# Kernel optimization log

Measured on AMD Instinct MI355X. Metric: run time of the kernel, lower is better.

The kernel has to match this reference:

```python
import jax, jax.numpy as jnp
import numpy as np

BS, SEQ, IN, H = 16, 1024, 512, 512


def setup_inputs() -> dict:
    key = jax.random.key(0)
    ks = jax.random.split(key, 10)
    std = 1.0 / np.sqrt(H)
    u = lambda k, shape: jax.random.uniform(k, shape, jnp.float32, -std, std)
    return {
        "x": jax.random.normal(ks[0], (BS, SEQ, IN), jnp.float32),
        # input projection fc: input_size -> hidden_size
        "Wfc": u(ks[1], (IN, H)),
        "bfc": u(ks[2], (H,)),
        # cell 1 (main hidden stream h): tree of matmuls + gated elementwise
        "W1x": u(ks[3], (2 * H, H)),  # layer-0 cells see duplicated features (2H)
        "W1h": u(ks[4], (H, H)),
        "W1g": u(ks[5], (H, H)),
        # cell 2 (second hidden stream c)
        "W2x": u(ks[6], (2 * H, H)),
        "W2h": u(ks[7], (H, H)),
        "W2g": u(ks[8], (H, H)),
    }


def reference(x, Wfc, bfc, W1x, W1h, W1g, W2x, W2h, W2g):
    bs = x.shape[0]
    # layer-0 input prep: fc projection then feature duplication (cat([x,x],dim=2))
    xp = x @ Wfc + bfc                      # [bs, seq, H]
    xp = jnp.concatenate([xp, xp], axis=-1)  # [bs, seq, 2H]
    xs = jnp.swapaxes(xp, 0, 1)             # [seq, bs, 2H] for scan over time

    h0 = jnp.zeros((bs, H), x.dtype)
    c0 = jnp.zeros((bs, H), x.dtype)

    def step(carry, x_t):
        h, c = carry  # hidden streams x2, x3 fed to each evolved cell
        h_new = jnp.tanh(x_t @ W1x + h @ W1h + jax.nn.sigmoid(c @ W1g) * h)
        c_new = jax.nn.sigmoid(x_t @ W2x + c @ W2h) * jnp.tanh(h @ W2g)
        return (h_new, c_new), h_new  # hidden_seq collects stream 0

    (h_fin, c_fin), hseq = jax.lax.scan(step, (h0, c0), xs)
    out = jnp.swapaxes(hseq, 0, 1)  # batch_first: [bs, seq, H]
    # final hidden states: [num_layers*(1), bs, H] per main stream
    return out, h_fin[None], c_fin[None]
```

## Files before the change

kernel.cpp:

```cpp
#include <hip/hip_runtime.h>


typedef unsigned short u16;
typedef unsigned int   u32;
typedef __attribute__((ext_vector_type(8))) short s8v;
typedef __attribute__((ext_vector_type(4))) float f4v;

__device__ __forceinline__ u16 f2bf_rne(float f){
  u32 u = __float_as_uint(f);
  u32 r = u + 0x7fffu + ((u >> 16) & 1u);
  return (u16)(r >> 16);
}
__device__ __forceinline__ float bf2f(u16 h){ return __uint_as_float(((u32)h) << 16); }
__device__ __forceinline__ f4v MFMA(s8v a, s8v b, f4v c){
  return __builtin_amdgcn_mfma_f32_16x16x32_bf16(a, b, c, 0, 0, 0);
}
__device__ __forceinline__ float sigmoidf_(float x){ return 1.0f / (1.0f + __expf(-x)); }
__device__ __forceinline__ float tanh_fast(float x){
  float e = __expf(2.0f * x);
  return 1.0f - 2.0f / (e + 1.0f);
}

template<bool CC> __device__ __forceinline__ s8v ld16(const u16* p){
  s8v r;
  if (CC) asm volatile("global_load_dwordx4 %0, %1, off sc0 sc1" : "=v"(r) : "v"(p));
  else    asm volatile("global_load_dwordx4 %0, %1, off"         : "=v"(r) : "v"(p));
  return r;
}
template<bool CC> __device__ __forceinline__ void st2(u16* p, u32 v){
  if (CC) asm volatile("global_store_short %0, %1, off sc0 sc1" :: "v"(p), "v"(v) : "memory");
  else    asm volatile("global_store_short %0, %1, off"         :: "v"(p), "v"(v) : "memory");
}
__device__ __forceinline__ void store_dword_cc(u32* p, u32 v){
  asm volatile("global_store_dword %0, %1, off sc0 sc1" :: "v"(p), "v"(v) : "memory");
}
__device__ __forceinline__ void store_dword_plain_wait(u32* p, u32 v){
  asm volatile("global_store_dword %0, %1, off\n\ts_waitcnt vmcnt(0)"
               :: "v"(p), "v"(v) : "memory");
}
__device__ __forceinline__ u32 load_dword_plain_wait(const u32* p){
  u32 r;
  asm volatile("global_load_dword %0, %1, off\n\ts_waitcnt vmcnt(0)"
               : "=v"(r) : "v"(p));
  return r;
}

#define SEQT 1024
#define NWG  16
#define PROT 16

static const size_t OFF_U1  = 0;
static const size_t OFF_U2  = 33554432;
static const size_t OFF_WCT = OFF_U2 + 16777216;
static const size_t OFF_ST  = OFF_WCT;
static const size_t OFF_WT  = OFF_WCT + 1048576;
static const size_t OFF_BC  = OFF_WT + 2097152;
static const size_t OFF_FL  = OFF_BC + 4096;
static const size_t OFF_TOK = OFF_FL + 65536;
static const size_t OFF_PRS = OFF_TOK + 4096;
static const size_t OFF_CTL = OFF_PRS + 4096;
static const size_t OFF_CN  = OFF_CTL + 4096;

__global__ void wcombk(const float* __restrict__ Wfc, const float* __restrict__ W1x,
                       const float* __restrict__ W2x, u16* __restrict__ Wct){
  __shared__ float A[16][17], B[16][17];
  const float* Wx = blockIdx.z ? W2x : W1x;
  int i0 = blockIdx.y * 16, n0 = blockIdx.x * 16;
  int tx = threadIdx.x, ty = threadIdx.y;
  float acc = 0.f;
  for (int kc = 0; kc < 512; kc += 16){
    A[ty][tx] = Wfc[(size_t)(i0 + ty) * 512 + kc + tx];
    B[ty][tx] = Wx[(size_t)(kc + ty) * 512 + n0 + tx]
              + Wx[(size_t)(kc + ty + 512) * 512 + n0 + tx];
    __syncthreads();
    #pragma unroll
    for (int kk = 0; kk < 16; ++kk) acc += A[ty][kk] * B[kk][tx];
    __syncthreads();
  }
  Wct[(size_t)(blockIdx.z * 512 + n0 + tx) * 512 + i0 + ty] = f2bf_rne(acc);
}

__global__ void bcombk(const float* __restrict__ bfc, const float* __restrict__ W1x,
                       const float* __restrict__ W2x, float* __restrict__ bc){
  int n = blockIdx.x * 256 + threadIdx.x;
  const float* Wx = (n < 512) ? W1x : W2x;
  int nl = n & 511;
  float acc = 0.f;
  for (int k = 0; k < 512; ++k)
    acc += bfc[k] * (Wx[(size_t)k * 512 + nl] + Wx[(size_t)(k + 512) * 512 + nl]);
  bc[n] = acc;
}

__global__ void wtk(const float* __restrict__ A, const float* __restrict__ B,
                    const float* __restrict__ C, const float* __restrict__ D,
                    u16* __restrict__ Wt){
  __shared__ float tile[32][33];
  const float* src = (blockIdx.z == 0) ? A : (blockIdx.z == 1) ? B
                    : (blockIdx.z == 2) ? C : D;
  int n0 = blockIdx.x * 32, k0 = blockIdx.y * 32;
  for (int i = threadIdx.y; i < 32; i += 8)
    tile[i][threadIdx.x] = src[(size_t)(k0 + i) * 512 + n0 + threadIdx.x];
  __syncthreads();
  for (int i = threadIdx.y; i < 32; i += 8)
    Wt[(size_t)blockIdx.z * 262144 + (size_t)(n0 + i) * 512 + k0 + threadIdx.x]
        = f2bf_rne(tile[threadIdx.x][i]);
}

__global__ __launch_bounds__(256) void gemmk(
    const float* __restrict__ x, const u16* __restrict__ Wct,
    const float* __restrict__ bc, float* __restrict__ U1, u16* __restrict__ U2){
  int l = threadIdx.x & 63, w = threadIdx.x >> 6;
  int lr = l & 15, lk = l >> 4;
  int m0 = blockIdx.y * 128 + (w & 1) * 64;
  int n0 = blockIdx.x * 64 + (w >> 1) * 32;
  f4v acc[4][2] = {};
  for (int ks = 0; ks < 16; ++ks){
    int k0 = ks * 32 + lk * 8;
    s8v bh0 = *(const s8v*)(Wct + (size_t)(n0 + lr) * 512 + k0);
    s8v bh1 = *(const s8v*)(Wct + (size_t)(n0 + 16 + lr) * 512 + k0);
    #pragma unroll
    for (int mi = 0; mi < 4; ++mi){
      const float* xp = x + (size_t)(m0 + mi * 16 + lr) * 512 + k0;
      f4v v0 = *(const f4v*)xp;
      f4v v1 = *(const f4v*)(xp + 4);
      s8v ah, al;
      #pragma unroll
      for (int j = 0; j < 4; ++j){
        { u32 u = __float_as_uint(v0[j]); ah[j] = (short)(u >> 16);
          float lof = v0[j] - __uint_as_float(u & 0xffff0000u);
          al[j] = (short)(__float_as_uint(lof) >> 16); }
        { u32 u = __float_as_uint(v1[j]); ah[j + 4] = (short)(u >> 16);
          float lof = v1[j] - __uint_as_float(u & 0xffff0000u);
          al[j + 4] = (short)(__float_as_uint(lof) >> 16); }
      }
      acc[mi][0] = MFMA(ah, bh0, acc[mi][0]);
      acc[mi][0] = MFMA(al, bh0, acc[mi][0]);
      acc[mi][1] = MFMA(ah, bh1, acc[mi][1]);
      acc[mi][1] = MFMA(al, bh1, acc[mi][1]);
    }
  }
  #pragma unroll
  for (int mi = 0; mi < 4; ++mi)
    #pragma unroll
    for (int ni = 0; ni < 2; ++ni){
      int n = n0 + ni * 16 + lr;
      float badd = bc[n];
      #pragma unroll
      for (int j = 0; j < 4; ++j){
        int r = m0 + mi * 16 + lk * 4 + j;
        int b = r >> 10, t = r & 1023;
        size_t oi = (size_t)(t * 16 + b) * 512;
        float v = acc[mi][ni][j] + badd;
        if (n < 512) U1[oi + n] = v;
        else         U2[oi + n - 512] = f2bf_rne(v);
      }
    }
}

template<bool CC>
__device__ __forceinline__ void scan_loop(
    int wg, int tid,
    const float* __restrict__ U1, const u16* __restrict__ U2,
    const u16* __restrict__ Wt, u16* __restrict__ st,
    u32* __restrict__ flags, u32* __restrict__ cnt,
    float* __restrict__ out, float* xg, float* xt){
  const int w = tid >> 6, l = tid & 63;
  const int lr = l & 15, lk = l >> 4;
  const int ncol0 = wg * 32 + lr;

  s8v bf0[16], bf1[16];
  {
    const u16* Wm = Wt + (size_t)w * (512 * 512);
    #pragma unroll
    for (int ks = 0; ks < 16; ++ks){
      bf0[ks] = *(const s8v*)(Wm + (size_t)ncol0 * 512 + ks * 32 + lk * 8);
      bf1[ks] = *(const s8v*)(Wm + (size_t)(ncol0 + 16) * 512 + ks * 32 + lk * 8);
    }
  }
  const bool useH = (w == 0) || (w == 3);
  float hp0[4] = {0, 0, 0, 0}, hp1[4] = {0, 0, 0, 0};
  long guard = 0;

  float un0[4], un1[4], uc0[4], uc1[4];
  u32   ur0[4], ur1[4];
  if (w == 0){
    #pragma unroll
    for (int j = 0; j < 4; ++j){
      size_t ro = (size_t)(lk * 4 + j) * 512;
      un0[j] = U1[ro + ncol0];
      un1[j] = U1[ro + ncol0 + 16];
    }
  } else if (w == 2){
    #pragma unroll
    for (int j = 0; j < 4; ++j){
      size_t ro = (size_t)(lk * 4 + j) * 512;
      ur0[j] = U2[ro + ncol0];
      ur1[j] = U2[ro + ncol0 + 16];
    }
  }

  for (int t = 0; t < SEQT; ++t){
    if (t > 0){
      if (CC){
        const u32* fl = flags + (size_t)(t - 1) * NWG;
        for (;;){
          u32 v = 1u;
          if (l < NWG) v = __hip_atomic_load(fl + l, __ATOMIC_RELAXED, __HIP_MEMORY_SCOPE_AGENT);
          if (__all(v != 0u)) break;
          if (++guard > 1000000L) break;
        }
      } else {
        if (w == 0){
          for (;;){
            u32 v = 0;
            if (l == 0)
              v = __hip_atomic_fetch_add(cnt + (t - 1), 0x10000u, __ATOMIC_RELAXED,
                                         __HIP_MEMORY_SCOPE_WORKGROUP);
            v = __builtin_amdgcn_readfirstlane(v);
            if ((v & 0xffffu) >= NWG) break;
            if (++guard > 8000000L) break;
          }
        }
        __syncthreads();
      }
      __builtin_amdgcn_sched_barrier(0);
    }
    u16* rb = st + (size_t)(t & (PROT - 1)) * 32768 + (useH ? 0 : 16384);
    s8v ah[16], al[16];
    {
      u16* bhp = rb + lr * 512 + lk * 8;
      u16* blp = rb + 8192 + lr * 512 + lk * 8;
      #pragma unroll
      for (int ks = 0; ks < 16; ++ks){
        ah[ks] = ld16<CC>(bhp + ks * 32);
        al[ks] = ld16<CC>(blp + ks * 32);
      }
    }
    asm volatile("s_waitcnt vmcnt(0)" ::: "memory");
    __builtin_amdgcn_sched_barrier(0);

    if (w == 0){
      #pragma unroll
      for (int j = 0; j < 4; ++j){ uc0[j] = un0[j]; uc1[j] = un1[j]; }
    } else if (w == 2){
      #pragma unroll
      for (int j = 0; j < 4; ++j){
        uc0[j] = __uint_as_float(ur0[j] << 16);
        uc1[j] = __uint_as_float(ur1[j] << 16);
      }
    }

    f4v a0 = {0, 0, 0, 0}, a1 = {0, 0, 0, 0};
    f4v b0 = {0, 0, 0, 0}, b1 = {0, 0, 0, 0};
    #pragma unroll
    for (int ks = 0; ks < 16; ++ks){
      a0 = MFMA(ah[ks], bf0[ks], a0);
      a1 = MFMA(ah[ks], bf1[ks], a1);
      b0 = MFMA(al[ks], bf0[ks], b0);
      b1 = MFMA(al[ks], bf1[ks], b1);
    }
    #pragma unroll
    for (int j = 0; j < 4; ++j){ a0[j] += b0[j]; a1[j] += b1[j]; }

    if (w == 1){
      #pragma unroll
      for (int j = 0; j < 4; ++j){
        xg[(0 * 16 + lk * 4 + j) * 16 + lr] = sigmoidf_(a0[j]);
        xg[(1 * 16 + lk * 4 + j) * 16 + lr] = sigmoidf_(a1[j]);
      }
    } else if (w == 3){
      #pragma unroll
      for (int j = 0; j < 4; ++j){
        xt[(0 * 16 + lk * 4 + j) * 16 + lr] = tanh_fast(a0[j]);
        xt[(1 * 16 + lk * 4 + j) * 16 + lr] = tanh_fast(a1[j]);
      }
    }
    __syncthreads();
    u16* wb = st + (size_t)((t + 1) & (PROT - 1)) * 32768;
    const int tn = (t + 1 < SEQT) ? t + 1 : t;
    float hn0v[4], hn1v[4], cn0v[4], cn1v[4];
    if (w == 0){
      #pragma unroll
      for (int j = 0; j < 4; ++j){
        int b = lk * 4 + j;
        float hn0 = tanh_fast(uc0[j] + a0[j] + xg[(0 * 16 + b) * 16 + lr] * hp0[j]);
        float hn1 = tanh_fast(uc1[j] + a1[j] + xg[(1 * 16 + b) * 16 + lr] * hp1[j]);
        hp0[j] = hn0; hp1[j] = hn1;
        hn0v[j] = hn0; hn1v[j] = hn1;
        u32 u0 = __float_as_uint(hn0), u1 = __float_as_uint(hn1);
        int bi = b * 512;
        st2<CC>(wb + bi + ncol0,      u0 >> 16);
        st2<CC>(wb + bi + ncol0 + 16, u1 >> 16);
        float lo0 = hn0 - __uint_as_float(u0 & 0xffff0000u);
        float lo1 = hn1 - __uint_as_float(u1 & 0xffff0000u);
        st2<CC>(wb + 8192 + bi + ncol0,      __float_as_uint(lo0) >> 16);
        st2<CC>(wb + 8192 + bi + ncol0 + 16, __float_as_uint(lo1) >> 16);
      }
      #pragma unroll
      for (int j = 0; j < 4; ++j){
        size_t ro = (size_t)(tn * 16 + lk * 4 + j) * 512;
        un0[j] = U1[ro + ncol0];
        un1[j] = U1[ro + ncol0 + 16];
      }
      asm volatile("s_waitcnt vmcnt(8)" ::: "memory");
    } else if (w == 2){
      #pragma unroll
      for (int j = 0; j < 4; ++j){
        int b = lk * 4 + j;
        float cn0 = sigmoidf_(uc0[j] + a0[j]) * xt[(0 * 16 + b) * 16 + lr];
        float cn1 = sigmoidf_(uc1[j] + a1[j]) * xt[(1 * 16 + b) * 16 + lr];
        cn0v[j] = cn0; cn1v[j] = cn1;
        u32 u0 = __float_as_uint(cn0), u1 = __float_as_uint(cn1);
        int bi = b * 512;
        st2<CC>(wb + 16384 + bi + ncol0,      u0 >> 16);
        st2<CC>(wb + 16384 + bi + ncol0 + 16, u1 >> 16);
        float lo0 = cn0 - __uint_as_float(u0 & 0xffff0000u);
        float lo1 = cn1 - __uint_as_float(u1 & 0xffff0000u);
        st2<CC>(wb + 24576 + bi + ncol0,      __float_as_uint(lo0) >> 16);
        st2<CC>(wb + 24576 + bi + ncol0 + 16, __float_as_uint(lo1) >> 16);
      }
      #pragma unroll
      for (int j = 0; j < 4; ++j){
        size_t ro = (size_t)(tn * 16 + lk * 4 + j) * 512;
        ur0[j] = U2[ro + ncol0];
        ur1[j] = U2[ro + ncol0 + 16];
      }
      asm volatile("s_waitcnt vmcnt(8)" ::: "memory");
    }
    __syncthreads();
    if (tid == 0){
      if (CC) store_dword_cc(flags + (size_t)t * NWG + wg, 1u);
      else    __hip_atomic_fetch_add(cnt + t, 1u, __ATOMIC_RELAXED,
                                     __HIP_MEMORY_SCOPE_WORKGROUP);
    }
    if (w == 0){
      #pragma unroll
      for (int j = 0; j < 4; ++j){
        int b = lk * 4 + j;
        size_t ob = (size_t)b * (SEQT * 512) + (size_t)t * 512;
        out[ob + ncol0]      = hn0v[j];
        out[ob + ncol0 + 16] = hn1v[j];
        if (t == SEQT - 1){
          out[8388608 + (size_t)b * 512 + ncol0]      = hn0v[j];
          out[8388608 + (size_t)b * 512 + ncol0 + 16] = hn1v[j];
        }
      }
    } else if (w == 2 && t == SEQT - 1){
      #pragma unroll
      for (int j = 0; j < 4; ++j){
        int b = lk * 4 + j;
        out[8396800 + (size_t)b * 512 + ncol0]      = cn0v[j];
        out[8396800 + (size_t)b * 512 + ncol0 + 16] = cn1v[j];
      }
    }
  }
}

__global__ __launch_bounds__(256, 1) void recurk(
    const float* __restrict__ U1, const u16* __restrict__ U2,
    const u16* __restrict__ Wt, u16* __restrict__ st,
    u32* __restrict__ flags, u32* __restrict__ cnt,
    u32* __restrict__ tok, u32* __restrict__ prs,
    u32* __restrict__ ctl, float* __restrict__ out){
  const int tid = threadIdx.x;
  __shared__ int slot_sh, mode_sh;
  __shared__ float xg[2 * 16 * 16], xt[2 * 16 * 16];
  u32* cntp  = ctl;
  u32* modep = ctl + 16;

  if (tid == 0){
    int s = -1;
    u32 xcc;
    asm volatile("s_getreg_b32 %0, hwreg(HW_REG_XCC_ID)" : "=s"(xcc));
    if ((xcc & 0xfu) == 0u)
      s = (int)__hip_atomic_fetch_add(cntp, 1u, __ATOMIC_RELAXED,
                                      __HIP_MEMORY_SCOPE_AGENT);
    slot_sh = s;
  }
  __syncthreads();
  const int slot = slot_sh;

  if (tid == 0){
    if (slot >= 0 && slot < NWG){
      store_dword_plain_wait(tok + slot * 16, 0x5A5A0000u + (u32)slot);
      __hip_atomic_store(prs + slot * 16, 1u, __ATOMIC_RELAXED,
                         __HIP_MEMORY_SCOPE_AGENT);
    }
    if (blockIdx.x == 0){
      long g = 0;
      for (;;){
        u32 c = __hip_atomic_load(cntp, __ATOMIC_RELAXED, __HIP_MEMORY_SCOPE_AGENT);
        if (c >= NWG) break;
        if (++g > 2000000L){ atomicCAS(modep, 0u, 2u); break; }
      }
    }
    if (slot == 0){
      bool ok = true;
      long g = 0;
      for (int s2 = 1; s2 < NWG && ok; ++s2){
        for (;;){
          u32 p = __hip_atomic_load(prs + s2 * 16, __ATOMIC_RELAXED,
                                    __HIP_MEMORY_SCOPE_AGENT);
          if (p) break;
          if (++g > 5000000L){ ok = false; break; }
        }
      }
      if (ok){
        for (int s2 = 1; s2 < NWG; ++s2){
          u32 v = load_dword_plain_wait(tok + s2 * 16);
          if (v != 0x5A5A0000u + (u32)s2){ ok = false; break; }
        }
      }
      atomicCAS(modep, 0u, ok ? 1u : 3u);
    }
    long g = 0;
    u32 m;
    for (;;){
      m = __hip_atomic_load(modep, __ATOMIC_RELAXED, __HIP_MEMORY_SCOPE_AGENT);
      if (m) break;
      if (++g > 50000000L){ m = 3u; break; }
    }
    mode_sh = (int)m;
  }
  __syncthreads();
  const int mode = mode_sh;

  int wg; bool part;
  if (mode == 2){ wg = blockIdx.x; part = (wg < NWG); }
  else          { wg = slot;       part = (slot >= 0 && slot < NWG); }
  if (!part) return;

  if (mode == 1) scan_loop<false>(wg, tid, U1, U2, Wt, st, flags, cnt, out, xg, xt);
  else           scan_loop<true >(wg, tid, U1, U2, Wt, st, flags, cnt, out, xg, xt);
}

extern "C" void kernel_launch(void* const* d_in, const int* in_sizes, int n_in,
                              void* d_out, int out_size, void* d_ws, size_t ws_size,
                              hipStream_t stream){
  const float* x   = (const float*)d_in[0];
  const float* Wfc = (const float*)d_in[1];
  const float* bfc = (const float*)d_in[2];
  const float* W1x = (const float*)d_in[3];
  const float* W1h = (const float*)d_in[4];
  const float* W1g = (const float*)d_in[5];
  const float* W2x = (const float*)d_in[6];
  const float* W2h = (const float*)d_in[7];
  const float* W2g = (const float*)d_in[8];

  char* ws = (char*)d_ws;
  float* U1   = (float*)(ws + OFF_U1);
  u16*   U2   = (u16*)  (ws + OFF_U2);
  u16*   Wct  = (u16*)  (ws + OFF_WCT);
  u16*   st   = (u16*)  (ws + OFF_ST);
  u16*   Wt   = (u16*)  (ws + OFF_WT);
  float* bc   = (float*)(ws + OFF_BC);
  u32*   flags= (u32*)  (ws + OFF_FL);
  u32*   tok  = (u32*)  (ws + OFF_TOK);
  u32*   prs  = (u32*)  (ws + OFF_PRS);
  u32*   ctl  = (u32*)  (ws + OFF_CTL);
  u32*   cnt  = (u32*)  (ws + OFF_CN);
  float* out  = (float*)d_out;

  hipMemsetAsync(ws + OFF_FL, 0, 65536 + 4096 + 4096 + 4096 + 4096, stream);

  wcombk<<<dim3(32, 32, 2), dim3(16, 16), 0, stream>>>(Wfc, W1x, W2x, Wct);
  bcombk<<<dim3(4), dim3(256), 0, stream>>>(bfc, W1x, W2x, bc);
  wtk   <<<dim3(16, 16, 4), dim3(32, 8), 0, stream>>>(W1h, W1g, W2h, W2g, Wt);
  gemmk <<<dim3(16, 128), dim3(256), 0, stream>>>(x, Wct, bc, U1, U2);
  hipMemsetAsync(ws + OFF_ST, 0, 1048576, stream);
  recurk<<<dim3(256), dim3(256), 0, stream>>>(U1, U2, Wt, st, flags, cnt, tok, prs, ctl, out);
}
```

Measured before the change: 6.445 ms.

## Split per-stream readiness flags and drop end-of-step block barrier in fast scan

```diff
diff --git a/kernel.cpp b/kernel.cpp
--- a/kernel.cpp
+++ b/kernel.cpp
@@ -60,6 +60,8 @@
 static const size_t OFF_PRS = OFF_TOK + 4096;
 static const size_t OFF_CTL = OFF_PRS + 4096;
 static const size_t OFF_CN  = OFF_CTL + 4096;
+static const size_t OFF_HF2 = OFF_CN + 4096;
+static const size_t OFF_CF2 = OFF_HF2 + 1048576;
 
 __global__ void wcombk(const float* __restrict__ Wfc, const float* __restrict__ W1x,
                        const float* __restrict__ W2x, u16* __restrict__ Wct){
@@ -157,12 +159,11 @@
     }
 }
 
-template<bool CC>
-__device__ __forceinline__ void scan_loop(
+__device__ __forceinline__ void scan_fast(
     int wg, int tid,
     const float* __restrict__ U1, const u16* __restrict__ U2,
     const u16* __restrict__ Wt, u16* __restrict__ st,
-    u32* __restrict__ flags, u32* __restrict__ cnt,
+    u32* __restrict__ hfl, u32* __restrict__ cfl,
     float* __restrict__ out, float* xg, float* xt){
   const int w = tid >> 6, l = tid & 63;
   const int lr = l & 15, lk = l >> 4;
@@ -178,8 +179,8 @@
     }
   }
   const bool useH = (w == 0) || (w == 3);
+  u32* myfl = useH ? hfl : cfl;
   float hp0[4] = {0, 0, 0, 0}, hp1[4] = {0, 0, 0, 0};
-  long guard = 0;
 
   float un0[4], un1[4], uc0[4], uc1[4];
   u32   ur0[4], ur1[4];
@@ -201,27 +202,17 @@
 
   for (int t = 0; t < SEQT; ++t){
     if (t > 0){
-      if (CC){
-        const u32* fl = flags + (size_t)(t - 1) * NWG;
-        for (;;){
-          u32 v = 1u;
-          if (l < NWG) v = __hip_atomic_load(fl + l, __ATOMIC_RELAXED, __HIP_MEMORY_SCOPE_AGENT);
-          if (__all(v != 0u)) break;
-          if (++guard > 1000000L) break;
+      u32* fl = myfl + (size_t)(t - 1) * (NWG * 16);
+      u32 seen = (l < NWG) ? 0u : 1u;
+      int g2 = 0;
+      for (;;){
+        if (!seen){
+          u32 v = __hip_atomic_fetch_add(fl + l * 16, 0x10000u,
+                                         __ATOMIC_RELAXED, __HIP_MEMORY_SCOPE_WORKGROUP);
+          if ((v & 0xffffu) != 0u) seen = 1u;
         }
-      } else {
-        if (w == 0){
-          for (;;){
-            u32 v = 0;
-            if (l == 0)
-              v = __hip_atomic_fetch_add(cnt + (t - 1), 0x10000u, __ATOMIC_RELAXED,
-                                         __HIP_MEMORY_SCOPE_WORKGROUP);
-            v = __builtin_amdgcn_readfirstlane(v);
-            if ((v & 0xffffu) >= NWG) break;
-            if (++guard > 8000000L) break;
-          }
-        }
-        __syncthreads();
+        if (__all(seen != 0u)) break;
+        if (++g2 > 2000000) break;
       }
       __builtin_amdgcn_sched_barrier(0);
     }
@@ -232,8 +223,8 @@
       u16* blp = rb + 8192 + lr * 512 + lk * 8;
       #pragma unroll
       for (int ks = 0; ks < 16; ++ks){
-        ah[ks] = ld16<CC>(bhp + ks * 32);
-        al[ks] = ld16<CC>(blp + ks * 32);
+        ah[ks] = ld16<false>(bhp + ks * 32);
+        al[ks] = ld16<false>(blp + ks * 32);
       }
     }
     asm volatile("s_waitcnt vmcnt(0)" ::: "memory");
@@ -262,39 +253,40 @@
     #pragma unroll
     for (int j = 0; j < 4; ++j){ a0[j] += b0[j]; a1[j] += b1[j]; }
 
+    const int par = t & 1;
     if (w == 1){
       #pragma unroll
       for (int j = 0; j < 4; ++j){
-        xg[(0 * 16 + lk * 4 + j) * 16 + lr] = sigmoidf_(a0[j]);
-        xg[(1 * 16 + lk * 4 + j) * 16 + lr] = sigmoidf_(a1[j]);
+        xg[((par * 2 + 0) * 16 + lk * 4 + j) * 16 + lr] = sigmoidf_(a0[j]);
+        xg[((par * 2 + 1) * 16 + lk * 4 + j) * 16 + lr] = sigmoidf_(a1[j]);
       }
     } else if (w == 3){
       #pragma unroll
       for (int j = 0; j < 4; ++j){
-        xt[(0 * 16 + lk * 4 + j) * 16 + lr] = tanh_fast(a0[j]);
-        xt[(1 * 16 + lk * 4 + j) * 16 + lr] = tanh_fast(a1[j]);
+        xt[((par * 2 + 0) * 16 + lk * 4 + j) * 16 + lr] = tanh_fast(a0[j]);
+        xt[((par * 2 + 1) * 16 + lk * 4 + j) * 16 + lr] = tanh_fast(a1[j]);
       }
     }
     __syncthreads();
     u16* wb = st + (size_t)((t + 1) & (PROT - 1)) * 32768;
     const int tn = (t + 1 < SEQT) ? t + 1 : t;
-    float hn0v[4], hn1v[4], cn0v[4], cn1v[4];
     if (w == 0){
+      float hn0v[4], hn1v[4];
       #pragma unroll
       for (int j = 0; j < 4; ++j){
         int b = lk * 4 + j;
-        float hn0 = tanh_fast(uc0[j] + a0[j] + xg[(0 * 16 + b) * 16 + lr] * hp0[j]);
-        float hn1 = tanh_fast(uc1[j] + a1[j] + xg[(1 * 16 + b) * 16 + lr] * hp1[j]);
+        float hn0 = tanh_fast(uc0[j] + a0[j] + xg[((par * 2 + 0) * 16 + b) * 16 + lr] * hp0[j]);
+        float hn1 = tanh_fast(uc1[j] + a1[j] + xg[((par * 2 + 1) * 16 + b) * 16 + lr] * hp1[j]);
         hp0[j] = hn0; hp1[j] = hn1;
         hn0v[j] = hn0; hn1v[j] = hn1;
         u32 u0 = __float_as_uint(hn0), u1 = __float_as_uint(hn1);
         int bi = b * 512;
-        st2<CC>(wb + bi + ncol0,      u0 >> 16);
-        st2<CC>(wb + bi + ncol0 + 16, u1 >> 16);
+        st2<false>(wb + bi + ncol0,      u0 >> 16);
+        st2<false>(wb + bi + ncol0 + 16, u1 >> 16);
         float lo0 = hn0 - __uint_as_float(u0 & 0xffff0000u);
         float lo1 = hn1 - __uint_as_float(u1 & 0xffff0000u);
-        st2<CC>(wb + 8192 + bi + ncol0,      __float_as_uint(lo0) >> 16);
-        st2<CC>(wb + 8192 + bi + ncol0 + 16, __float_as_uint(lo1) >> 16);
+        st2<false>(wb + 8192 + bi + ncol0,      __float_as_uint(lo0) >> 16);
+        st2<false>(wb + 8192 + bi + ncol0 + 16, __float_as_uint(lo1) >> 16);
       }
       #pragma unroll
       for (int j = 0; j < 4; ++j){
@@ -303,37 +295,9 @@
         un1[j] = U1[ro + ncol0 + 16];
       }
       asm volatile("s_waitcnt vmcnt(8)" ::: "memory");
-    } else if (w == 2){
-      #pragma unroll
-      for (int j = 0; j < 4; ++j){
-        int b = lk * 4 + j;
-        float cn0 = sigmoidf_(uc0[j] + a0[j]) * xt[(0 * 16 + b) * 16 + lr];
-        float cn1 = sigmoidf_(uc1[j] + a1[j]) * xt[(1 * 16 + b) * 16 + lr];
-        cn0v[j] = cn0; cn1v[j] = cn1;
-        u32 u0 = __float_as_uint(cn0), u1 = __float_as_uint(cn1);
-        int bi = b * 512;
-        st2<CC>(wb + 16384 + bi + ncol0,      u0 >> 16);
-        st2<CC>(wb + 16384 + bi + ncol0 + 16, u1 >> 16);
-        float lo0 = cn0 - __uint_as_float(u0 & 0xffff0000u);
-        float lo1 = cn1 - __uint_as_float(u1 & 0xffff0000u);
-        st2<CC>(wb + 24576 + bi + ncol0,      __float_as_uint(lo0) >> 16);
-        st2<CC>(wb + 24576 + bi + ncol0 + 16, __float_as_uint(lo1) >> 16);
-      }
-      #pragma unroll
-      for (int j = 0; j < 4; ++j){
-        size_t ro = (size_t)(tn * 16 + lk * 4 + j) * 512;
-        ur0[j] = U2[ro + ncol0];
-        ur1[j] = U2[ro + ncol0 + 16];
-      }
-      asm volatile("s_waitcnt vmcnt(8)" ::: "memory");
-    }
-    __syncthreads();
-    if (tid == 0){
-      if (CC) store_dword_cc(flags + (size_t)t * NWG + wg, 1u);
-      else    __hip_atomic_fetch_add(cnt + t, 1u, __ATOMIC_RELAXED,
-                                     __HIP_MEMORY_SCOPE_WORKGROUP);
-    }
-    if (w == 0){
+      if (l == 0)
+        __hip_atomic_fetch_add(hfl + (size_t)t * (NWG * 16) + wg * 16, 1u,
+                               __ATOMIC_RELAXED, __HIP_MEMORY_SCOPE_WORKGROUP);
       #pragma unroll
       for (int j = 0; j < 4; ++j){
         int b = lk * 4 + j;
@@ -345,6 +309,182 @@
           out[8388608 + (size_t)b * 512 + ncol0 + 16] = hn1v[j];
         }
       }
+    } else if (w == 2){
+      float cn0v[4], cn1v[4];
+      #pragma unroll
+      for (int j = 0; j < 4; ++j){
+        int b = lk * 4 + j;
+        float cn0 = sigmoidf_(uc0[j] + a0[j]) * xt[((par * 2 + 0) * 16 + b) * 16 + lr];
+        float cn1 = sigmoidf_(uc1[j] + a1[j]) * xt[((par * 2 + 1) * 16 + b) * 16 + lr];
+        cn0v[j] = cn0; cn1v[j] = cn1;
+        u32 u0 = __float_as_uint(cn0), u1 = __float_as_uint(cn1);
+        int bi = b * 512;
+        st2<false>(wb + 16384 + bi + ncol0,      u0 >> 16);
+        st2<false>(wb + 16384 + bi + ncol0 + 16, u1 >> 16);
+        float lo0 = cn0 - __uint_as_float(u0 & 0xffff0000u);
+        float lo1 = cn1 - __uint_as_float(u1 & 0xffff0000u);
+        st2<false>(wb + 24576 + bi + ncol0,      __float_as_uint(lo0) >> 16);
+        st2<false>(wb + 24576 + bi + ncol0 + 16, __float_as_uint(lo1) >> 16);
+      }
+      #pragma unroll
+      for (int j = 0; j < 4; ++j){
+        size_t ro = (size_t)(tn * 16 + lk * 4 + j) * 512;
+        ur0[j] = U2[ro + ncol0];
+        ur1[j] = U2[ro + ncol0 + 16];
+      }
+      asm volatile("s_waitcnt vmcnt(8)" ::: "memory");
+      if (l == 0)
+        __hip_atomic_fetch_add(cfl + (size_t)t * (NWG * 16) + wg * 16, 1u,
+                               __ATOMIC_RELAXED, __HIP_MEMORY_SCOPE_WORKGROUP);
+      if (t == SEQT - 1){
+        #pragma unroll
+        for (int j = 0; j < 4; ++j){
+          int b = lk * 4 + j;
+          out[8396800 + (size_t)b * 512 + ncol0]      = cn0v[j];
+          out[8396800 + (size_t)b * 512 + ncol0 + 16] = cn1v[j];
+        }
+      }
+    }
+  }
+}
+
+__device__ __forceinline__ void scan_cc(
+    int wg, int tid,
+    const float* __restrict__ U1, const u16* __restrict__ U2,
+    const u16* __restrict__ Wt, u16* __restrict__ st,
+    u32* __restrict__ flags, float* __restrict__ out, float* xg, float* xt){
+  const int w = tid >> 6, l = tid & 63;
+  const int lr = l & 15, lk = l >> 4;
+  const int ncol0 = wg * 32 + lr;
+  s8v bf0[16], bf1[16];
+  {
+    const u16* Wm = Wt + (size_t)w * (512 * 512);
+    #pragma unroll
+    for (int ks = 0; ks < 16; ++ks){
+      bf0[ks] = *(const s8v*)(Wm + (size_t)ncol0 * 512 + ks * 32 + lk * 8);
+      bf1[ks] = *(const s8v*)(Wm + (size_t)(ncol0 + 16) * 512 + ks * 32 + lk * 8);
+    }
+  }
+  const bool useH = (w == 0) || (w == 3);
+  float hp0[4] = {0, 0, 0, 0}, hp1[4] = {0, 0, 0, 0};
+  long guard = 0;
+  for (int t = 0; t < SEQT; ++t){
+    float uu0[4], uu1[4];
+    if (w == 0){
+      #pragma unroll
+      for (int j = 0; j < 4; ++j){
+        size_t ro = (size_t)(t * 16 + lk * 4 + j) * 512;
+        uu0[j] = U1[ro + ncol0];
+        uu1[j] = U1[ro + ncol0 + 16];
+      }
+    } else if (w == 2){
+      #pragma unroll
+      for (int j = 0; j < 4; ++j){
+        size_t ro = (size_t)(t * 16 + lk * 4 + j) * 512;
+        uu0[j] = bf2f(U2[ro + ncol0]);
+        uu1[j] = bf2f(U2[ro + ncol0 + 16]);
+      }
+    }
+    if (t > 0){
+      const u32* fl = flags + (size_t)(t - 1) * NWG;
+      for (;;){
+        u32 v = 1u;
+        if (l < NWG) v = __hip_atomic_load(fl + l, __ATOMIC_RELAXED, __HIP_MEMORY_SCOPE_AGENT);
+        if (__all(v != 0u)) break;
+        if (++guard > 1000000L) break;
+      }
+      __builtin_amdgcn_sched_barrier(0);
+    }
+    u16* rb = st + (size_t)(t & (PROT - 1)) * 32768 + (useH ? 0 : 16384);
+    s8v ah[16], al[16];
+    {
+      u16* bhp = rb + lr * 512 + lk * 8;
+      u16* blp = rb + 8192 + lr * 512 + lk * 8;
+      #pragma unroll
+      for (int ks = 0; ks < 16; ++ks){
+        ah[ks] = ld16<true>(bhp + ks * 32);
+        al[ks] = ld16<true>(blp + ks * 32);
+      }
+    }
+    asm volatile("s_waitcnt vmcnt(0)" ::: "memory");
+    __builtin_amdgcn_sched_barrier(0);
+    f4v a0 = {0, 0, 0, 0}, a1 = {0, 0, 0, 0};
+    f4v b0 = {0, 0, 0, 0}, b1 = {0, 0, 0, 0};
+    #pragma unroll
+    for (int ks = 0; ks < 16; ++ks){
+      a0 = MFMA(ah[ks], bf0[ks], a0);
+      a1 = MFMA(ah[ks], bf1[ks], a1);
+      b0 = MFMA(al[ks], bf0[ks], b0);
+      b1 = MFMA(al[ks], bf1[ks], b1);
+    }
+    #pragma unroll
+    for (int j = 0; j < 4; ++j){ a0[j] += b0[j]; a1[j] += b1[j]; }
+    if (w == 1){
+      #pragma unroll
+      for (int j = 0; j < 4; ++j){
+        xg[(0 * 16 + lk * 4 + j) * 16 + lr] = sigmoidf_(a0[j]);
+        xg[(1 * 16 + lk * 4 + j) * 16 + lr] = sigmoidf_(a1[j]);
+      }
+    } else if (w == 3){
+      #pragma unroll
+      for (int j = 0; j < 4; ++j){
+        xt[(0 * 16 + lk * 4 + j) * 16 + lr] = tanh_fast(a0[j]);
+        xt[(1 * 16 + lk * 4 + j) * 16 + lr] = tanh_fast(a1[j]);
+      }
+    }
+    __syncthreads();
+    u16* wb = st + (size_t)((t + 1) & (PROT - 1)) * 32768;
+    float hn0v[4], hn1v[4], cn0v[4], cn1v[4];
+    if (w == 0){
+      #pragma unroll
+      for (int j = 0; j < 4; ++j){
+        int b = lk * 4 + j;
+        float hn0 = tanh_fast(uu0[j] + a0[j] + xg[(0 * 16 + b) * 16 + lr] * hp0[j]);
+        float hn1 = tanh_fast(uu1[j] + a1[j] + xg[(1 * 16 + b) * 16 + lr] * hp1[j]);
+        hp0[j] = hn0; hp1[j] = hn1;
+        hn0v[j] = hn0; hn1v[j] = hn1;
+        u32 u0 = __float_as_uint(hn0), u1 = __float_as_uint(hn1);
+        int bi = b * 512;
+        st2<true>(wb + bi + ncol0,      u0 >> 16);
+        st2<true>(wb + bi + ncol0 + 16, u1 >> 16);
+        float lo0 = hn0 - __uint_as_float(u0 & 0xffff0000u);
+        float lo1 = hn1 - __uint_as_float(u1 & 0xffff0000u);
+        st2<true>(wb + 8192 + bi + ncol0,      __float_as_uint(lo0) >> 16);
+        st2<true>(wb + 8192 + bi + ncol0 + 16, __float_as_uint(lo1) >> 16);
+      }
+      asm volatile("s_waitcnt vmcnt(0)" ::: "memory");
+    } else if (w == 2){
+      #pragma unroll
+      for (int j = 0; j < 4; ++j){
+        int b = lk * 4 + j;
+        float cn0 = sigmoidf_(uu0[j] + a0[j]) * xt[(0 * 16 + b) * 16 + lr];
+        float cn1 = sigmoidf_(uu1[j] + a1[j]) * xt[(1 * 16 + b) * 16 + lr];
+        cn0v[j] = cn0; cn1v[j] = cn1;
+        u32 u0 = __float_as_uint(cn0), u1 = __float_as_uint(cn1);
+        int bi = b * 512;
+        st2<true>(wb + 16384 + bi + ncol0,      u0 >> 16);
+        st2<true>(wb + 16384 + bi + ncol0 + 16, u1 >> 16);
+        float lo0 = cn0 - __uint_as_float(u0 & 0xffff0000u);
+        float lo1 = cn1 - __uint_as_float(u1 & 0xffff0000u);
+        st2<true>(wb + 24576 + bi + ncol0,      __float_as_uint(lo0) >> 16);
+        st2<true>(wb + 24576 + bi + ncol0 + 16, __float_as_uint(lo1) >> 16);
+      }
+      asm volatile("s_waitcnt vmcnt(0)" ::: "memory");
+    }
+    __syncthreads();
+    if (tid == 0) store_dword_cc(flags + (size_t)t * NWG + wg, 1u);
+    if (w == 0){
+      #pragma unroll
+      for (int j = 0; j < 4; ++j){
+        int b = lk * 4 + j;
+        size_t ob = (size_t)b * (SEQT * 512) + (size_t)t * 512;
+        out[ob + ncol0]      = hn0v[j];
+        out[ob + ncol0 + 16] = hn1v[j];
+        if (t == SEQT - 1){
+          out[8388608 + (size_t)b * 512 + ncol0]      = hn0v[j];
+          out[8388608 + (size_t)b * 512 + ncol0 + 16] = hn1v[j];
+        }
+      }
     } else if (w == 2 && t == SEQT - 1){
       #pragma unroll
       for (int j = 0; j < 4; ++j){
@@ -359,12 +499,12 @@
 __global__ __launch_bounds__(256, 1) void recurk(
     const float* __restrict__ U1, const u16* __restrict__ U2,
     const u16* __restrict__ Wt, u16* __restrict__ st,
-    u32* __restrict__ flags, u32* __restrict__ cnt,
+    u32* __restrict__ flags, u32* __restrict__ hfl, u32* __restrict__ cfl,
     u32* __restrict__ tok, u32* __restrict__ prs,
     u32* __restrict__ ctl, float* __restrict__ out){
   const int tid = threadIdx.x;
   __shared__ int slot_sh, mode_sh;
-  __shared__ float xg[2 * 16 * 16], xt[2 * 16 * 16];
+  __shared__ float xg[4 * 16 * 16], xt[4 * 16 * 16];
   u32* cntp  = ctl;
   u32* modep = ctl + 16;
 
@@ -430,8 +570,8 @@
   else          { wg = slot;       part = (slot >= 0 && slot < NWG); }
   if (!part) return;
 
-  if (mode == 1) scan_loop<false>(wg, tid, U1, U2, Wt, st, flags, cnt, out, xg, xt);
-  else           scan_loop<true >(wg, tid, U1, U2, Wt, st, flags, cnt, out, xg, xt);
+  if (mode == 1) scan_fast(wg, tid, U1, U2, Wt, st, hfl, cfl, out, xg, xt);
+  else           scan_cc (wg, tid, U1, U2, Wt, st, flags, out, xg, xt);
 }
 
 extern "C" void kernel_launch(void* const* d_in, const int* in_sizes, int n_in,
@@ -458,15 +598,17 @@
   u32*   tok  = (u32*)  (ws + OFF_TOK);
   u32*   prs  = (u32*)  (ws + OFF_PRS);
   u32*   ctl  = (u32*)  (ws + OFF_CTL);
-  u32*   cnt  = (u32*)  (ws + OFF_CN);
+  u32*   hfl  = (u32*)  (ws + OFF_HF2);
+  u32*   cfl  = (u32*)  (ws + OFF_CF2);
   float* out  = (float*)d_out;
 
   hipMemsetAsync(ws + OFF_FL, 0, 65536 + 4096 + 4096 + 4096 + 4096, stream);
+  hipMemsetAsync(ws + OFF_HF2, 0, 2097152, stream);
 
   wcombk<<<dim3(32, 32, 2), dim3(16, 16), 0, stream>>>(Wfc, W1x, W2x, Wct);
   bcombk<<<dim3(4), dim3(256), 0, stream>>>(bfc, W1x, W2x, bc);
   wtk   <<<dim3(16, 16, 4), dim3(32, 8), 0, stream>>>(W1h, W1g, W2h, W2g, Wt);
   gemmk <<<dim3(16, 128), dim3(256), 0, stream>>>(x, Wct, bc, U1, U2);
   hipMemsetAsync(ws + OFF_ST, 0, 1048576, stream);
-  recurk<<<dim3(256), dim3(256), 0, stream>>>(U1, U2, Wt, st, flags, cnt, tok, prs, ctl, out);
-}
+  recurk<<<dim3(256), dim3(256), 0, stream>>>(U1, U2, Wt, st, flags, hfl, cfl, tok, prs, ctl, out);
+}
```

New measurement: 7.268 ms. 12.8% more time.
